# Performance work log

Measured on AMD Instinct MI355X. Metric: run time of the kernel, lower is better.

Reference implementation:

```python
import jax, jax.numpy as jnp
import numpy as np

B, L_IN, L_OUT, N, COV, EMB, H = 32, 336, 48, 512, 4, 32, 64
C = 1 + COV
D_IN = EMB + COV


def setup_inputs() -> dict:
    key = jax.random.key(0)
    ks = jax.random.split(key, 16)
    s = 1.0 / np.sqrt(H)

    def rn(k, shape, scale):
        return jax.random.normal(k, shape, jnp.float32) * scale

    return {
        "history_data": jax.random.normal(ks[0], (B, L_IN, N, C), jnp.float32),
        "future_data": jax.random.normal(ks[1], (B, L_OUT, N, C), jnp.float32),
        "emb_W": rn(ks[2], (EMB, 1), 0.5),
        "emb_b": rn(ks[3], (EMB,), 0.1),
        "W_ih0": rn(ks[4], (4 * H, D_IN), s),
        "W_hh0": rn(ks[5], (4 * H, H), s),
        "b_ih0": rn(ks[6], (4 * H,), s),
        "b_hh0": rn(ks[7], (4 * H,), s),
        "W_ih1": rn(ks[8], (4 * H, H), s),
        "W_hh1": rn(ks[9], (4 * H, H), s),
        "b_ih1": rn(ks[10], (4 * H,), s),
        "b_hh1": rn(ks[11], (4 * H,), s),
        "head_W": rn(ks[12], (2, H), s),
        "head_b": rn(ks[13], (2,), 0.1),
        "train": 1,
    }


def _lstm_cell(x_t, h, c, W_ih, W_hh, b_ih, b_hh):
    # gate order i, f, g, o (torch nn.LSTM convention)
    g = x_t @ W_ih.T + b_ih + h @ W_hh.T + b_hh
    i, f, gg, o = jnp.split(g, 4, axis=-1)
    c = jax.nn.sigmoid(f) * c + jax.nn.sigmoid(i) * jnp.tanh(gg)
    h = jax.nn.sigmoid(o) * jnp.tanh(c)
    return h, c


def _deepar_forward(history_data, future_data, emb_W, emb_b,
                    W_ih0, W_hh0, b_ih0, b_hh0,
                    W_ih1, W_hh1, b_ih1, b_hh1,
                    head_W, head_b):
    Bb, L_in, Nn, _ = history_data.shape
    L_out = future_data.shape[1]
    # [B, L_in+L_out, N, .]
    target = jnp.concatenate([history_data[..., 0:1], future_data[..., 0:1]], axis=1)
    covar = jnp.concatenate([history_data[..., 1:], future_data[..., 1:]], axis=1)
    # train=True branch: teacher forcing for t = 1 .. L-1
    prev = target[:, :-1]        # [B, T, N, 1]
    cov_t = covar[:, 1:]         # [B, T, N, COV]
    emb = prev @ emb_W.T + emb_b  # [B, T, N, EMB]
    x = jnp.concatenate([emb, cov_t], axis=-1)      # [B, T, N, EMB+COV]
    T = x.shape[1]
    x = x.transpose(1, 0, 2, 3).reshape(T, Bb * Nn, -1)  # scan over time
    Hh = W_hh0.shape[1]
    z = jnp.zeros((Bb * Nn, Hh), x.dtype)

    def step(carry, x_t):
        h0, c0, h1, c1 = carry
        h0, c0 = _lstm_cell(x_t, h0, c0, W_ih0, W_hh0, b_ih0, b_hh0)
        h1, c1 = _lstm_cell(h0, h1, c1, W_ih1, W_hh1, b_ih1, b_hh1)
        p = jax.nn.relu(h1) @ head_W.T + head_b       # [BN, 2]
        mu = p[:, 0:1]
        sigma = jax.nn.softplus(p[:, 1:2])
        return (h0, c0, h1, c1), jnp.concatenate([mu, sigma], axis=-1)

    _, outs = jax.lax.scan(step, (z, z, z, z), x)     # [T, BN, 2]
    outs = outs.reshape(T, Bb, Nn, 2).transpose(1, 0, 2, 3)  # [B, T, N, 2]
    return outs[:, -L_out:]


def reference(history_data, future_data, emb_W, emb_b,
              W_ih0, W_hh0, b_ih0, b_hh0,
              W_ih1, W_hh1, b_ih1, b_hh1,
              head_W, head_b, train):
    # train is a static Python int (1 = teacher forcing branch implemented here)
    return _deepar_forward(history_data, future_data, emb_W, emb_b,
                           W_ih0, W_hh0, b_ih0, b_hh0,
                           W_ih1, W_hh1, b_ih1, b_hh1,
                           head_W, head_b)
```

## Files before the change

### kernel.cpp

```cpp
#include <hip/hip_runtime.h>


#define T_STEPS 383
#define AST 232
#define LOG2E 1.44269504088896340736f

typedef __attribute__((ext_vector_type(8))) short short8;
typedef __attribute__((ext_vector_type(2))) unsigned int uint2v;
typedef __attribute__((ext_vector_type(4))) float floatx4;

__device__ __forceinline__ unsigned short f2bf(float f){
  union { float f; unsigned u; } v; v.f = f;
  unsigned u = v.u + 0x7fffu + ((v.u >> 16) & 1u);
  return (unsigned short)(u >> 16);
}
__device__ __forceinline__ unsigned short f2bf_fast(float f){
  union { float f; unsigned u; } v; v.f = f;
  return (unsigned short)((v.u + 0x8000u) >> 16);
}
__device__ __forceinline__ float bf2f(unsigned short b){
  union { unsigned u; float f; } v; v.u = ((unsigned)b) << 16; return v.f;
}

__device__ __forceinline__ float lstm_h(float iv, float fv, float gv, float ov, float& c){
  const float ea = __builtin_amdgcn_exp2f(-fv);
  const float eb = __builtin_amdgcn_exp2f(-iv);
  const float ec = __builtin_amdgcn_exp2f(-gv);
  const float eo = __builtin_amdgcn_exp2f(-ov);
  const float A = 1.f + ea, B = 1.f + eb, C = 1.f + ec, D = 1.f + eo;
  const float BC = B * C;
  const float num = c * BC + A * (2.f - C);
  const float cn = num * __builtin_amdgcn_rcpf(A * BC);
  c = cn;
  const float arg = fminf(cn * (-2.f * LOG2E), 126.f);
  const float E = 1.f + __builtin_amdgcn_exp2f(arg);
  return (2.f - E) * __builtin_amdgcn_rcpf(D * E);
}

__global__ __launch_bounds__(256, 2) void deepar_kernel(
    const float* __restrict__ hist, const float* __restrict__ fut,
    const float* __restrict__ embW, const float* __restrict__ embB,
    const float* __restrict__ Wih0, const float* __restrict__ Whh0,
    const float* __restrict__ bih0, const float* __restrict__ bhh0,
    const float* __restrict__ Wih1, const float* __restrict__ Whh1,
    const float* __restrict__ bih1, const float* __restrict__ bhh1,
    const float* __restrict__ headW, const float* __restrict__ headB,
    float* __restrict__ outp)
{
  const int tid  = threadIdx.x;
  const int lane = tid & 63;
  const int wv   = tid >> 6;
  const int l15  = lane & 15;
  const int quad = lane >> 4;
  const int koff = quad * 8;
  const int jcol  = wv * 16 + l15;
  const int jbase = wv * 16 + quad * 4;

  const int b  = blockIdx.x >> 4;
  const int n0 = (blockIdx.x & 15) * 32;

  __shared__ __align__(16) unsigned short A[32 * AST];
  __shared__ __align__(16) unsigned short W1[256 * 128];
  __shared__ float HW[128];

  for (int i = tid; i < 32 * AST; i += 256) A[i] = 0;
  if (tid < 128) HW[tid] = headW[tid];
  __syncthreads();
  if (tid < 32){
    A[tid * AST + 133] = 0x3f80;
    A[tid * AST + 134] = 0x3f80;
  }
  const float hb0 = headB[0], hb1 = headB[1];

  short8 bf0[4][3];
  float  bi1[4];
  #pragma unroll
  for (int g = 0; g < 4; ++g){
    const float gsc = (g == 2) ? 2.f * LOG2E : LOG2E;
    const int r = g * 64 + wv * 16 + l15;
    float u = 0.f, bb = bih0[r] + bhh0[r];
    #pragma unroll
    for (int e = 0; e < 32; ++e){
      float wval = Wih0[r * 36 + e];
      u  += wval * embW[e];
      bb += wval * embB[e];
    }
    const float bbs = bb * gsc;
    const unsigned short bbq = f2bf(bbs);
    const float bbr = bbs - bf2f(bbq);
    bi1[g] = (bih1[r] + bhh1[r]) * gsc;
    #pragma unroll
    for (int kf = 0; kf < 2; ++kf)
      #pragma unroll
      for (int j = 0; j < 8; ++j)
        bf0[g][kf][j] = (short)f2bf(Whh0[r * 64 + kf * 32 + koff + j] * gsc);
    #pragma unroll
    for (int j = 0; j < 8; ++j){
      int kk = koff + j;
      unsigned short q16;
      if (kk == 5)      q16 = bbq;
      else if (kk == 6) q16 = f2bf(bbr);
      else {
        float v = 0.f;
        if (kk == 0) v = u;
        else if (kk >= 1 && kk <= 4) v = Wih0[r * 36 + 32 + (kk - 1)];
        q16 = f2bf(v * gsc);
      }
      bf0[g][2][j] = (short)q16;
    }
    #pragma unroll
    for (int kf = 0; kf < 4; ++kf){
      const float* src = (kf < 2) ? (Wih1 + r * 64 + kf * 32)
                                  : (Whh1 + r * 64 + (kf - 2) * 32);
      short8 w;
      #pragma unroll
      for (int j = 0; j < 8; ++j)
        w[j] = (short)f2bf(src[koff + j] * gsc);
      *(short8*)&W1[(((wv * 16 + g * 4 + kf) * 64) + lane) * 8] = w;
    }
  }

  const bool isPrev = (tid < 32);
  const bool isCov  = (tid >= 64 && tid < 192);
  int ss = 0, cc = 0;
  if (isPrev){ ss = tid; cc = 0; }
  if (isCov) { ss = (tid - 64) >> 2; cc = 1 + ((tid - 64) & 3); }
  const int myN = n0 + ss;

  auto loadSlab = [&](int tt) -> float {
    if (isPrev){
      int l = tt; if (l > 383) l = 383;
      return (l < 336) ? hist[(((size_t)b * 336 + l) * 512 + myN) * 5]
                       : fut [(((size_t)b * 48 + (l - 336)) * 512 + myN) * 5];
    } else if (isCov){
      int l = tt + 1; if (l > 383) l = 383;
      return (l < 336) ? hist[(((size_t)b * 336 + l) * 512 + myN) * 5 + cc]
                       : fut [(((size_t)b * 48 + (l - 336)) * 512 + myN) * 5 + cc];
    }
    return 0.f;
  };

  float rCur = loadSlab(0);
  if (isPrev || isCov) A[ss * AST + 128 + cc] = f2bf(rCur);
  rCur = loadSlab(1);

  float c0s[8], c1s[8];
  #pragma unroll
  for (int i = 0; i < 8; ++i){ c0s[i] = 0.f; c1s[i] = 0.f; }

  const int hd_hs   = tid >> 3;
  const int hd_outc = (tid >> 2) & 1;
  const int hd_part = tid & 3;

  auto headOp = [&](int tt, int reg){
    const short8 hv0 = *(const short8*)&A[hd_hs * AST + reg + hd_part * 16];
    const short8 hv1 = *(const short8*)&A[hd_hs * AST + reg + hd_part * 16 + 8];
    float p = 0.f;
    #pragma unroll
    for (int jj = 0; jj < 8; ++jj){
      float a0 = fmaxf(bf2f((unsigned short)hv0[jj]), 0.f);
      float a1 = fmaxf(bf2f((unsigned short)hv1[jj]), 0.f);
      p += a0 * HW[hd_outc * 64 + hd_part * 16 + jj];
      p += a1 * HW[hd_outc * 64 + hd_part * 16 + 8 + jj];
    }
    p += __shfl_xor(p, 1);
    p += __shfl_xor(p, 2);
    if ((tid & 3) == 0){
      float val;
      if (hd_outc == 0) val = p + hb0;
      else {
        float x = p + hb1;
        val = fmaxf(x, 0.f) + __logf(1.f + __expf(-fabsf(x)));
      }
      outp[(((size_t)b * 48 + (tt - 335)) * 512 + (n0 + hd_hs)) * 2 + hd_outc] = val;
    }
  };

  if (((blockIdx.x >> 3) & 1) && wv == 0){
    float z = 1.5f + (float)lane;
    for (int i = 0; i < 300; ++i)
      asm volatile("v_exp_f32 %0, %1" : "=v"(z) : "v"(z));
    (void)z;
  }

  __syncthreads();

  for (int t = 0; t < T_STEPS; ++t){
    const int h1rd = (t & 1) ? 64 : 144;
    const int h1wr = (t & 1) ? 144 : 64;

    const float rNxt = loadSlab(t + 2);

    floatx4 acc[4][2];
    #pragma unroll
    for (int g = 0; g < 4; ++g)
      #pragma unroll
      for (int mt = 0; mt < 2; ++mt){
        floatx4 z = {0.f, 0.f, 0.f, 0.f};
        acc[g][mt] = z;
      }
    const int c0off[3] = { 0, 32, 128 };
    #pragma unroll
    for (int mt = 0; mt < 2; ++mt){
      #pragma unroll
      for (int kf = 0; kf < 3; ++kf){
        short8 af = *(const short8*)&A[(mt * 16 + l15) * AST + c0off[kf] + koff];
        #pragma unroll
        for (int g = 0; g < 4; ++g)
          acc[g][mt] = __builtin_amdgcn_mfma_f32_16x16x32_bf16(bf0[g][kf], af, acc[g][mt], 0, 0, 0);
      }
    }
    float hn[8];
    #pragma unroll
    for (int mt = 0; mt < 2; ++mt)
      #pragma unroll
      for (int q = 0; q < 4; ++q){
        int idx = mt * 4 + q;
        hn[idx] = lstm_h(acc[0][mt][q], acc[1][mt][q], acc[2][mt][q], acc[3][mt][q], c0s[idx]);
      }
    asm volatile("s_barrier" ::: "memory");
    #pragma unroll
    for (int mt = 0; mt < 2; ++mt){
      uint2v pk;
      asm("v_cvt_pk_bf16_f32 %0, %1, %2" : "=v"(pk.x) : "v"(hn[mt*4+0]), "v"(hn[mt*4+1]));
      asm("v_cvt_pk_bf16_f32 %0, %1, %2" : "=v"(pk.y) : "v"(hn[mt*4+2]), "v"(hn[mt*4+3]));
      *(uint2v*)&A[(mt * 16 + l15) * AST + jbase] = pk;
    }
    if (isPrev || isCov) A[ss * AST + 128 + cc] = f2bf_fast(rCur);
    if (t >= 336) headOp(t - 1, h1rd);
    rCur = rNxt;
    asm volatile("s_waitcnt lgkmcnt(0)\n\ts_barrier" ::: "memory");

    #pragma unroll
    for (int g = 0; g < 4; ++g)
      #pragma unroll
      for (int mt = 0; mt < 2; ++mt){
        floatx4 binit = { bi1[g], bi1[g], bi1[g], bi1[g] };
        acc[g][mt] = binit;
      }
    const int c1off[4] = { 0, 32, h1rd, h1rd + 32 };
    #pragma unroll
    for (int kf = 0; kf < 4; ++kf){
      short8 wfr[4];
      #pragma unroll
      for (int g = 0; g < 4; ++g)
        wfr[g] = *(const short8*)&W1[(((wv * 16 + g * 4 + kf) * 64) + lane) * 8];
      #pragma unroll
      for (int mt = 0; mt < 2; ++mt){
        short8 af = *(const short8*)&A[(mt * 16 + l15) * AST + c1off[kf] + koff];
        #pragma unroll
        for (int g = 0; g < 4; ++g)
          acc[g][mt] = __builtin_amdgcn_mfma_f32_16x16x32_bf16(af, wfr[g], acc[g][mt], 0, 0, 0);
      }
    }
    #pragma unroll
    for (int mt = 0; mt < 2; ++mt)
      #pragma unroll
      for (int q = 0; q < 4; ++q){
        int idx = mt * 4 + q;
        hn[idx] = lstm_h(acc[0][mt][q], acc[1][mt][q], acc[2][mt][q], acc[3][mt][q], c1s[idx]);
      }
    #pragma unroll
    for (int mt = 0; mt < 2; ++mt)
      #pragma unroll
      for (int q = 0; q < 4; ++q){
        int s = mt * 16 + quad * 4 + q;
        A[s * AST + h1wr + jcol] = f2bf_fast(hn[mt * 4 + q]);
      }
  }

  __syncthreads();
  headOp(382, 64);
}

extern "C" void kernel_launch(void* const* d_in, const int* in_sizes, int n_in,
                              void* d_out, int out_size, void* d_ws, size_t ws_size,
                              hipStream_t stream) {
  (void)in_sizes; (void)n_in; (void)out_size; (void)d_ws; (void)ws_size;
  deepar_kernel<<<dim3(512), dim3(256), 0, stream>>>(
      (const float*)d_in[0],  (const float*)d_in[1],
      (const float*)d_in[2],  (const float*)d_in[3],
      (const float*)d_in[4],  (const float*)d_in[5],
      (const float*)d_in[6],  (const float*)d_in[7],
      (const float*)d_in[8],  (const float*)d_in[9],
      (const float*)d_in[10], (const float*)d_in[11],
      (const float*)d_in[12], (const float*)d_in[13],
      (float*)d_out);
}
```

Before: 1.194 ms.

## Pipeline LSTM layers across wave groups with 64-series blocks

```diff
diff --git a/kernel.cpp b/kernel.cpp
--- a/kernel.cpp
+++ b/kernel.cpp
@@ -1,8 +1,8 @@
 #include <hip/hip_runtime.h>
 
 
-#define T_STEPS 383
-#define AST 232
+#define AST 272
+#define NPH 385
 #define LOG2E 1.44269504088896340736f
 
 typedef __attribute__((ext_vector_type(8))) short short8;
@@ -37,7 +37,7 @@
   return (2.f - E) * __builtin_amdgcn_rcpf(D * E);
 }
 
-__global__ __launch_bounds__(256, 2) void deepar_kernel(
+__global__ __launch_bounds__(512, 2) void deepar_kernel(
     const float* __restrict__ hist, const float* __restrict__ fut,
     const float* __restrict__ embW, const float* __restrict__ embB,
     const float* __restrict__ Wih0, const float* __restrict__ Whh0,
@@ -53,75 +53,83 @@
   const int l15  = lane & 15;
   const int quad = lane >> 4;
   const int koff = quad * 8;
-  const int jcol  = wv * 16 + l15;
-  const int jbase = wv * 16 + quad * 4;
-
-  const int b  = blockIdx.x >> 4;
-  const int n0 = (blockIdx.x & 15) * 32;
-
-  __shared__ __align__(16) unsigned short A[32 * AST];
-  __shared__ __align__(16) unsigned short W1[256 * 128];
+  const bool isL0 = (wv < 4);
+  const int jt    = wv & 3;
+  const int jbase = jt * 16 + quad * 4;
+
+  const int b  = blockIdx.x >> 3;
+  const int n0 = (blockIdx.x & 7) * 64;
+
+  __shared__ __align__(16) unsigned short A[64 * AST];
+  __shared__ __align__(16) unsigned short W1[64 * 64 * 8];
   __shared__ float HW[128];
 
-  for (int i = tid; i < 32 * AST; i += 256) A[i] = 0;
+  for (int i = tid; i < 64 * AST; i += 512) A[i] = 0;
   if (tid < 128) HW[tid] = headW[tid];
   __syncthreads();
-  if (tid < 32){
-    A[tid * AST + 133] = 0x3f80;
-    A[tid * AST + 134] = 0x3f80;
+  if (tid < 64){
+    A[tid * AST + 261] = 0x3f80;  A[tid * AST + 262] = 0x3f80;
+    A[tid * AST + 269] = 0x3f80;  A[tid * AST + 270] = 0x3f80;
   }
   const float hb0 = headB[0], hb1 = headB[1];
 
-  short8 bf0[4][3];
-  float  bi1[4];
+  short8  bf0[4][3];
+  floatx4 bi1v[4];
   #pragma unroll
   for (int g = 0; g < 4; ++g){
     const float gsc = (g == 2) ? 2.f * LOG2E : LOG2E;
-    const int r = g * 64 + wv * 16 + l15;
-    float u = 0.f, bb = bih0[r] + bhh0[r];
-    #pragma unroll
-    for (int e = 0; e < 32; ++e){
-      float wval = Wih0[r * 36 + e];
-      u  += wval * embW[e];
-      bb += wval * embB[e];
-    }
-    const float bbs = bb * gsc;
-    const unsigned short bbq = f2bf(bbs);
-    const float bbr = bbs - bf2f(bbq);
-    bi1[g] = (bih1[r] + bhh1[r]) * gsc;
-    #pragma unroll
-    for (int kf = 0; kf < 2; ++kf)
-      #pragma unroll
-      for (int j = 0; j < 8; ++j)
-        bf0[g][kf][j] = (short)f2bf(Whh0[r * 64 + kf * 32 + koff + j] * gsc);
-    #pragma unroll
-    for (int j = 0; j < 8; ++j){
-      int kk = koff + j;
-      unsigned short q16;
-      if (kk == 5)      q16 = bbq;
-      else if (kk == 6) q16 = f2bf(bbr);
-      else {
-        float v = 0.f;
-        if (kk == 0) v = u;
-        else if (kk >= 1 && kk <= 4) v = Wih0[r * 36 + 32 + (kk - 1)];
-        q16 = f2bf(v * gsc);
-      }
-      bf0[g][2][j] = (short)q16;
-    }
-    #pragma unroll
-    for (int kf = 0; kf < 4; ++kf){
-      const float* src = (kf < 2) ? (Wih1 + r * 64 + kf * 32)
-                                  : (Whh1 + r * 64 + (kf - 2) * 32);
-      short8 w;
-      #pragma unroll
-      for (int j = 0; j < 8; ++j)
-        w[j] = (short)f2bf(src[koff + j] * gsc);
-      *(short8*)&W1[(((wv * 16 + g * 4 + kf) * 64) + lane) * 8] = w;
+    const int r = g * 64 + jt * 16 + l15;
+    if (isL0){
+      float u = 0.f, bb = bih0[r] + bhh0[r];
+      #pragma unroll
+      for (int e = 0; e < 32; ++e){
+        float wval = Wih0[r * 36 + e];
+        u  += wval * embW[e];
+        bb += wval * embB[e];
+      }
+      const float bbs = bb * gsc;
+      const unsigned short bbq = f2bf(bbs);
+      const float bbr = bbs - bf2f(bbq);
+      #pragma unroll
+      for (int kf = 0; kf < 2; ++kf)
+        #pragma unroll
+        for (int j = 0; j < 8; ++j)
+          bf0[g][kf][j] = (short)f2bf(Whh0[r * 64 + kf * 32 + koff + j] * gsc);
+      #pragma unroll
+      for (int j = 0; j < 8; ++j){
+        int kk = koff + j;
+        unsigned short q16;
+        if (kk == 5)      q16 = bbq;
+        else if (kk == 6) q16 = f2bf(bbr);
+        else {
+          float v = 0.f;
+          if (kk == 0) v = u;
+          else if (kk >= 1 && kk <= 4) v = Wih0[r * 36 + 32 + (kk - 1)];
+          q16 = f2bf(v * gsc);
+        }
+        bf0[g][2][j] = (short)q16;
+      }
+    } else {
+      #pragma unroll
+      for (int q = 0; q < 4; ++q){
+        const int re = g * 64 + jt * 16 + quad * 4 + q;
+        bi1v[g][q] = (bih1[re] + bhh1[re]) * gsc;
+      }
+      #pragma unroll
+      for (int kf = 0; kf < 4; ++kf){
+        const float* src = (kf < 2) ? (Wih1 + r * 64 + kf * 32)
+                                    : (Whh1 + r * 64 + (kf - 2) * 32);
+        short8 w;
+        #pragma unroll
+        for (int j = 0; j < 8; ++j)
+          w[j] = (short)f2bf(src[koff + j] * gsc);
+        *(short8*)&W1[(((jt * 16 + g * 4 + kf) * 64) + lane) * 8] = w;
+      }
     }
   }
 
-  const bool isPrev = (tid < 32);
-  const bool isCov  = (tid >= 64 && tid < 192);
+  const bool isPrev = (tid < 64);
+  const bool isCov  = (tid >= 64 && tid < 320);
   int ss = 0, cc = 0;
   if (isPrev){ ss = tid; cc = 0; }
   if (isCov) { ss = (tid - 64) >> 2; cc = 1 + ((tid - 64) & 3); }
@@ -141,143 +149,136 @@
   };
 
   float rCur = loadSlab(0);
-  if (isPrev || isCov) A[ss * AST + 128 + cc] = f2bf(rCur);
+  if (isPrev || isCov) A[ss * AST + 256 + cc] = f2bf(rCur);
   rCur = loadSlab(1);
 
-  float c0s[8], c1s[8];
+  float cst[16];
   #pragma unroll
-  for (int i = 0; i < 8; ++i){ c0s[i] = 0.f; c1s[i] = 0.f; }
+  for (int i = 0; i < 16; ++i) cst[i] = 0.f;
 
   const int hd_hs   = tid >> 3;
   const int hd_outc = (tid >> 2) & 1;
   const int hd_part = tid & 3;
 
-  auto headOp = [&](int tt, int reg){
-    const short8 hv0 = *(const short8*)&A[hd_hs * AST + reg + hd_part * 16];
-    const short8 hv1 = *(const short8*)&A[hd_hs * AST + reg + hd_part * 16 + 8];
-    float p = 0.f;
-    #pragma unroll
-    for (int jj = 0; jj < 8; ++jj){
-      float a0 = fmaxf(bf2f((unsigned short)hv0[jj]), 0.f);
-      float a1 = fmaxf(bf2f((unsigned short)hv1[jj]), 0.f);
-      p += a0 * HW[hd_outc * 64 + hd_part * 16 + jj];
-      p += a1 * HW[hd_outc * 64 + hd_part * 16 + 8 + jj];
-    }
-    p += __shfl_xor(p, 1);
-    p += __shfl_xor(p, 2);
-    if ((tid & 3) == 0){
-      float val;
-      if (hd_outc == 0) val = p + hb0;
-      else {
-        float x = p + hb1;
-        val = fmaxf(x, 0.f) + __logf(1.f + __expf(-fabsf(x)));
-      }
-      outp[(((size_t)b * 48 + (tt - 335)) * 512 + (n0 + hd_hs)) * 2 + hd_outc] = val;
-    }
-  };
-
-  if (((blockIdx.x >> 3) & 1) && wv == 0){
-    float z = 1.5f + (float)lane;
-    for (int i = 0; i < 300; ++i)
-      asm volatile("v_exp_f32 %0, %1" : "=v"(z) : "v"(z));
-    (void)z;
-  }
-
   __syncthreads();
 
-  for (int t = 0; t < T_STEPS; ++t){
-    const int h1rd = (t & 1) ? 64 : 144;
-    const int h1wr = (t & 1) ? 144 : 64;
-
-    const float rNxt = loadSlab(t + 2);
-
-    floatx4 acc[4][2];
-    #pragma unroll
-    for (int g = 0; g < 4; ++g)
-      #pragma unroll
-      for (int mt = 0; mt < 2; ++mt){
-        floatx4 z = {0.f, 0.f, 0.f, 0.f};
-        acc[g][mt] = z;
-      }
-    const int c0off[3] = { 0, 32, 128 };
-    #pragma unroll
-    for (int mt = 0; mt < 2; ++mt){
-      #pragma unroll
-      for (int kf = 0; kf < 3; ++kf){
-        short8 af = *(const short8*)&A[(mt * 16 + l15) * AST + c0off[kf] + koff];
+  for (int p = 0; p < NPH; ++p){
+    const int par = p & 1;
+    const float rNxt = loadSlab(p + 2);
+    if (isPrev || isCov)
+      A[ss * AST + 256 + (par ^ 1) * 8 + cc] = f2bf_fast(rCur);
+
+    const int h0rd = (par ^ 1) * 64;
+
+    if (isL0){
+      if (p < 383){
+        const int h0wr = par * 64;
+        const int xrd  = 256 + par * 8;
+        floatx4 acc[4][4];
         #pragma unroll
         for (int g = 0; g < 4; ++g)
-          acc[g][mt] = __builtin_amdgcn_mfma_f32_16x16x32_bf16(bf0[g][kf], af, acc[g][mt], 0, 0, 0);
-      }
-    }
-    float hn[8];
-    #pragma unroll
-    for (int mt = 0; mt < 2; ++mt)
-      #pragma unroll
-      for (int q = 0; q < 4; ++q){
-        int idx = mt * 4 + q;
-        hn[idx] = lstm_h(acc[0][mt][q], acc[1][mt][q], acc[2][mt][q], acc[3][mt][q], c0s[idx]);
-      }
-    asm volatile("s_barrier" ::: "memory");
-    #pragma unroll
-    for (int mt = 0; mt < 2; ++mt){
-      uint2v pk;
-      asm("v_cvt_pk_bf16_f32 %0, %1, %2" : "=v"(pk.x) : "v"(hn[mt*4+0]), "v"(hn[mt*4+1]));
-      asm("v_cvt_pk_bf16_f32 %0, %1, %2" : "=v"(pk.y) : "v"(hn[mt*4+2]), "v"(hn[mt*4+3]));
-      *(uint2v*)&A[(mt * 16 + l15) * AST + jbase] = pk;
-    }
-    if (isPrev || isCov) A[ss * AST + 128 + cc] = f2bf_fast(rCur);
-    if (t >= 336) headOp(t - 1, h1rd);
+          #pragma unroll
+          for (int mt = 0; mt < 4; ++mt){
+            floatx4 z = {0.f, 0.f, 0.f, 0.f};
+            acc[g][mt] = z;
+          }
+        const int c0off[3] = { h0rd, h0rd + 32, xrd };
+        #pragma unroll
+        for (int mt = 0; mt < 4; ++mt){
+          #pragma unroll
+          for (int kf = 0; kf < 3; ++kf){
+            short8 af = *(const short8*)&A[(mt * 16 + l15) * AST + c0off[kf] + koff];
+            #pragma unroll
+            for (int g = 0; g < 4; ++g)
+              acc[g][mt] = __builtin_amdgcn_mfma_f32_16x16x32_bf16(bf0[g][kf], af, acc[g][mt], 0, 0, 0);
+          }
+        }
+        #pragma unroll
+        for (int mt = 0; mt < 4; ++mt){
+          float hn[4];
+          #pragma unroll
+          for (int q = 0; q < 4; ++q)
+            hn[q] = lstm_h(acc[0][mt][q], acc[1][mt][q], acc[2][mt][q], acc[3][mt][q], cst[mt * 4 + q]);
+          uint2v pk;
+          asm("v_cvt_pk_bf16_f32 %0, %1, %2" : "=v"(pk.x) : "v"(hn[0]), "v"(hn[1]));
+          asm("v_cvt_pk_bf16_f32 %0, %1, %2" : "=v"(pk.y) : "v"(hn[2]), "v"(hn[3]));
+          *(uint2v*)&A[(mt * 16 + l15) * AST + h0wr + jbase] = pk;
+        }
+      }
+    } else {
+      if (p >= 1 && p < 384){
+        const int h1rd = 128 + par * 64;
+        const int h1wr = 128 + (par ^ 1) * 64;
+        floatx4 acc[4][4];
+        #pragma unroll
+        for (int g = 0; g < 4; ++g)
+          #pragma unroll
+          for (int mt = 0; mt < 4; ++mt)
+            acc[g][mt] = bi1v[g];
+        const int c1off[4] = { h0rd, h0rd + 32, h1rd, h1rd + 32 };
+        #pragma unroll
+        for (int kf = 0; kf < 4; ++kf){
+          short8 wfr[4];
+          #pragma unroll
+          for (int g = 0; g < 4; ++g)
+            wfr[g] = *(const short8*)&W1[(((jt * 16 + g * 4 + kf) * 64) + lane) * 8];
+          #pragma unroll
+          for (int mt = 0; mt < 4; ++mt){
+            short8 af = *(const short8*)&A[(mt * 16 + l15) * AST + c1off[kf] + koff];
+            #pragma unroll
+            for (int g = 0; g < 4; ++g)
+              acc[g][mt] = __builtin_amdgcn_mfma_f32_16x16x32_bf16(wfr[g], af, acc[g][mt], 0, 0, 0);
+          }
+        }
+        #pragma unroll
+        for (int mt = 0; mt < 4; ++mt){
+          float hn[4];
+          #pragma unroll
+          for (int q = 0; q < 4; ++q)
+            hn[q] = lstm_h(acc[0][mt][q], acc[1][mt][q], acc[2][mt][q], acc[3][mt][q], cst[mt * 4 + q]);
+          uint2v pk;
+          asm("v_cvt_pk_bf16_f32 %0, %1, %2" : "=v"(pk.x) : "v"(hn[0]), "v"(hn[1]));
+          asm("v_cvt_pk_bf16_f32 %0, %1, %2" : "=v"(pk.y) : "v"(hn[2]), "v"(hn[3]));
+          *(uint2v*)&A[(mt * 16 + l15) * AST + h1wr + jbase] = pk;
+        }
+      }
+    }
+
+    if (p >= 337){
+      const int hreg = 128 + par * 64;
+      const short8 hv0 = *(const short8*)&A[hd_hs * AST + hreg + hd_part * 16];
+      const short8 hv1 = *(const short8*)&A[hd_hs * AST + hreg + hd_part * 16 + 8];
+      float pv = 0.f;
+      #pragma unroll
+      for (int jj = 0; jj < 8; ++jj){
+        float a0 = fmaxf(bf2f((unsigned short)hv0[jj]), 0.f);
+        float a1 = fmaxf(bf2f((unsigned short)hv1[jj]), 0.f);
+        pv += a0 * HW[hd_outc * 64 + hd_part * 16 + jj];
+        pv += a1 * HW[hd_outc * 64 + hd_part * 16 + 8 + jj];
+      }
+      pv += __shfl_xor(pv, 1);
+      pv += __shfl_xor(pv, 2);
+      if ((tid & 3) == 0){
+        float val;
+        if (hd_outc == 0) val = pv + hb0;
+        else {
+          float x = pv + hb1;
+          val = fmaxf(x, 0.f) + __logf(1.f + __expf(-fabsf(x)));
+        }
+        outp[(((size_t)b * 48 + (p - 337)) * 512 + (n0 + hd_hs)) * 2 + hd_outc] = val;
+      }
+    }
+
     rCur = rNxt;
     asm volatile("s_waitcnt lgkmcnt(0)\n\ts_barrier" ::: "memory");
-
-    #pragma unroll
-    for (int g = 0; g < 4; ++g)
-      #pragma unroll
-      for (int mt = 0; mt < 2; ++mt){
-        floatx4 binit = { bi1[g], bi1[g], bi1[g], bi1[g] };
-        acc[g][mt] = binit;
-      }
-    const int c1off[4] = { 0, 32, h1rd, h1rd + 32 };
-    #pragma unroll
-    for (int kf = 0; kf < 4; ++kf){
-      short8 wfr[4];
-      #pragma unroll
-      for (int g = 0; g < 4; ++g)
-        wfr[g] = *(const short8*)&W1[(((wv * 16 + g * 4 + kf) * 64) + lane) * 8];
-      #pragma unroll
-      for (int mt = 0; mt < 2; ++mt){
-        short8 af = *(const short8*)&A[(mt * 16 + l15) * AST + c1off[kf] + koff];
-        #pragma unroll
-        for (int g = 0; g < 4; ++g)
-          acc[g][mt] = __builtin_amdgcn_mfma_f32_16x16x32_bf16(af, wfr[g], acc[g][mt], 0, 0, 0);
-      }
-    }
-    #pragma unroll
-    for (int mt = 0; mt < 2; ++mt)
-      #pragma unroll
-      for (int q = 0; q < 4; ++q){
-        int idx = mt * 4 + q;
-        hn[idx] = lstm_h(acc[0][mt][q], acc[1][mt][q], acc[2][mt][q], acc[3][mt][q], c1s[idx]);
-      }
-    #pragma unroll
-    for (int mt = 0; mt < 2; ++mt)
-      #pragma unroll
-      for (int q = 0; q < 4; ++q){
-        int s = mt * 16 + quad * 4 + q;
-        A[s * AST + h1wr + jcol] = f2bf_fast(hn[mt * 4 + q]);
-      }
   }
-
-  __syncthreads();
-  headOp(382, 64);
 }
 
 extern "C" void kernel_launch(void* const* d_in, const int* in_sizes, int n_in,
                               void* d_out, int out_size, void* d_ws, size_t ws_size,
                               hipStream_t stream) {
   (void)in_sizes; (void)n_in; (void)out_size; (void)d_ws; (void)ws_size;
-  deepar_kernel<<<dim3(512), dim3(256), 0, stream>>>(
+  deepar_kernel<<<dim3(256), dim3(512), 0, stream>>>(
       (const float*)d_in[0],  (const float*)d_in[1],
       (const float*)d_in[2],  (const float*)d_in[3],
       (const float*)d_in[4],  (const float*)d_in[5],
```

Measured after the change: 1.294 ms. 8.4% more time.
